# Kernel optimization log

Measured on AMD Instinct MI355X. Metric: run time of the kernel, lower is better.

## Reference

```python
import jax, jax.numpy as jnp
import numpy as np

N = 100000   # nodes
E = 1600000  # edges
IN = 512     # in_channels
H = 256      # hidden_channels
C = 40       # out_channels
BITS = 8     # INT8 fake quantization


def fake_quant(x, bits=BITS):
    """Symmetric per-tensor quantize-dequantize with straight-through estimator."""
    qmax = float(2 ** (bits - 1) - 1)
    scale = jnp.max(jnp.abs(x)) / qmax + 1e-12
    q = jnp.clip(jnp.round(x / scale), -qmax - 1.0, qmax) * scale
    # STE: forward = q, backward = identity
    return x + jax.lax.stop_gradient(q - x)


def quant_linear(x, w, b):
    # LinearQuantized: fake-quant inputs and weights, fp accumulate
    return fake_quant(x) @ fake_quant(w).T + b


def gcn_propagate(x, edge_index):
    """Symmetric-normalized sparse propagation: out = D^-1/2 A D^-1/2 x."""
    src, dst = edge_index[0], edge_index[1]
    deg = jax.ops.segment_sum(jnp.ones((E,), x.dtype), dst, num_segments=N)
    dinv = jnp.where(deg > 0, jax.lax.rsqrt(jnp.maximum(deg, 1.0)), 0.0)
    coef = dinv[src] * dinv[dst]                     # [E]
    msgs = x[src] * coef[:, None]                    # [E, C]
    return jax.ops.segment_sum(msgs, dst, num_segments=N)  # [N, C]


def setup_inputs() -> dict:
    key = jax.random.key(0)
    ks = jax.random.split(key, 6)
    x = jax.random.normal(ks[0], (N, IN), jnp.float32)
    edge_index = jax.random.randint(ks[1], (2, E), 0, N, dtype=jnp.int32)
    w1 = jax.random.normal(ks[2], (H, IN), jnp.float32) * (1.0 / np.sqrt(IN))
    b1 = jnp.zeros((H,), jnp.float32)
    w2 = jax.random.normal(ks[3], (C, H), jnp.float32) * (1.0 / np.sqrt(H))
    b2 = jnp.zeros((C,), jnp.float32)
    return {"x": x, "edge_index": edge_index, "w1": w1, "b1": b1, "w2": w2, "b2": b2}


def reference(x, edge_index, w1, b1, w2, b2):
    # dropout: identity in eval mode
    h = jax.nn.relu(quant_linear(x, w1, b1))         # [N, H]
    z = quant_linear(h, w2, b2)                      # [N, C]
    z = gcn_propagate(z, edge_index)                 # [N, C]
    return jax.nn.log_softmax(z, axis=1)
```

## Files before the change

### kernel.cpp

```cpp
#include <hip/hip_runtime.h>
#include <hip/hip_bf16.h>
#include <hip/hip_fp16.h>
#include <stdint.h>
#include <stddef.h>

#define NN   100000
#define NE   1600000
#define INC  512
#define HID  256
#define OC   40
#define OCP  48

#define LDS1 144
#define LDSB2 272

#define NBKT ((NN + 255) / 256)
#define NMT1 ((NN + 127) / 128)
#define GEMM1_BLKS (((NMT1 + 7) / 8) * 16)

#define ABS_X_BLKS  2048
#define ABS_W1_BLKS 128
#define ABS_W2_BLKS 16
#define ABS_TOT     (ABS_X_BLKS + ABS_W1_BLKS + ABS_W2_BLKS)
#define CHIST_BLKS  256
#define QW1_BLKS    128
#define QW2_BLKS    16
#define QW_TOT      (QW1_BLKS + QW2_BLKS)
#define BIN_BLOCKS  400
#define BIN_EPB     (NE / BIN_BLOCKS)

typedef float  f32x4  __attribute__((ext_vector_type(4)));
typedef int    i32x4  __attribute__((ext_vector_type(4)));
typedef _Float16 f16x8 __attribute__((ext_vector_type(8)));

__device__ unsigned g_amax_bits[4];
__device__ float    g_dinv[NN];
__device__ signed char g_qw1[HID * INC];
__device__ signed char g_qw2[OCP * HID];
__device__ _Float16 g_h[(size_t)NN * HID];
__device__ float    g_z[(size_t)NN * OC];
__device__ unsigned g_chist[NBKT];
__device__ unsigned g_cstart[NBKT + 1];
__device__ unsigned g_ccur[NBKT];
__device__ uint2    g_bin[NE];
__device__ unsigned g_rowstart[NN + 1];
__device__ int      g_csr_src[NE];

__device__ __forceinline__ float quantf(float v, float rs) {
    return fminf(fmaxf(rintf(v * rs), -128.0f), 127.0f);
}
__device__ __forceinline__ int pack4(float a, float b, float c, float d, float rs) {
    int q0 = (int)quantf(a, rs), q1 = (int)quantf(b, rs);
    int q2 = (int)quantf(c, rs), q3 = (int)quantf(d, rs);
    return (q0 & 255) | ((q1 & 255) << 8) | ((q2 & 255) << 16) | ((q3 & 255) << 24);
}
__device__ __forceinline__ i32x4 loadpack16(const float* p, float rs) {
    f32x4 v0 = *(const f32x4*)(p);
    f32x4 v1 = *(const f32x4*)(p + 4);
    f32x4 v2 = *(const f32x4*)(p + 8);
    f32x4 v3 = *(const f32x4*)(p + 12);
    i32x4 o;
    o[0] = pack4(v0.x, v0.y, v0.z, v0.w, rs);
    o[1] = pack4(v1.x, v1.y, v1.z, v1.w, rs);
    o[2] = pack4(v2.x, v2.y, v2.z, v2.w, rs);
    o[3] = pack4(v3.x, v3.y, v3.z, v3.w, rs);
    return o;
}

__global__ void init_kernel() {
    int idx = blockIdx.x * blockDim.x + threadIdx.x;
    int stride = gridDim.x * blockDim.x;
    for (int i = idx; i < NBKT; i += stride) g_chist[i] = 0u;
    for (int i = idx; i < (OCP * HID) / 4; i += stride) ((int*)g_qw2)[i] = 0;
    if (idx < 4) g_amax_bits[idx] = 0u;
}

__global__ void __launch_bounds__(256) absmax_chist_kernel(const float* __restrict__ x,
                                                           const float* __restrict__ w1,
                                                           const float* __restrict__ w2,
                                                           const int* __restrict__ ei) {
    __shared__ unsigned shist[NBKT];
    __shared__ float sm[4];
    int b = blockIdx.x;
    int t = threadIdx.x;
    if (b < ABS_TOT) {
        const float* src; int n4, slot, bbase, nb;
        if (b < ABS_X_BLKS) {
            src = x;  n4 = (NN * INC) / 4;  slot = 0; bbase = 0;                       nb = ABS_X_BLKS;
        } else if (b < ABS_X_BLKS + ABS_W1_BLKS) {
            src = w1; n4 = (HID * INC) / 4; slot = 1; bbase = ABS_X_BLKS;              nb = ABS_W1_BLKS;
        } else {
            src = w2; n4 = (OC * HID) / 4;  slot = 2; bbase = ABS_X_BLKS + ABS_W1_BLKS; nb = ABS_W2_BLKS;
        }
        int idx = (b - bbase) * 256 + t;
        int stride = nb * 256;
        const f32x4* s4 = (const f32x4*)src;
        float m = 0.0f;
        for (int i = idx; i < n4; i += stride) {
            f32x4 v = s4[i];
            m = fmaxf(m, fmaxf(fmaxf(fabsf(v.x), fabsf(v.y)),
                               fmaxf(fabsf(v.z), fabsf(v.w))));
        }
#pragma unroll
        for (int off = 32; off > 0; off >>= 1) m = fmaxf(m, __shfl_xor(m, off, 64));
        if ((t & 63) == 0) sm[t >> 6] = m;
        __syncthreads();
        if (t == 0) {
            float mm = fmaxf(fmaxf(sm[0], sm[1]), fmaxf(sm[2], sm[3]));
            atomicMax(&g_amax_bits[slot], __float_as_uint(mm));
        }
    } else {
        const int* dst = ei + NE;
        for (int i = t; i < NBKT; i += 256) shist[i] = 0u;
        __syncthreads();
        int idx = (b - ABS_TOT) * 256 + t;
        int stride = CHIST_BLKS * 256;
        for (int e = idx; e < NE; e += stride) atomicAdd(&shist[dst[e] >> 8], 1u);
        __syncthreads();
        for (int i = t; i < NBKT; i += 256) {
            unsigned c = shist[i];
            if (c) atomicAdd(&g_chist[i], c);
        }
    }
}

__global__ void cscan_kernel() {
    int t = threadIdx.x;
    unsigned v = (t < NBKT) ? g_chist[t] : 0u;
    int lane = t & 63, wv = t >> 6;
    unsigned sc = v;
#pragma unroll
    for (int off = 1; off < 64; off <<= 1) {
        unsigned n = __shfl_up(sc, off, 64);
        if (lane >= off) sc += n;
    }
    __shared__ unsigned ws[8];
    if (lane == 63) ws[wv] = sc;
    __syncthreads();
    unsigned woff = 0;
    for (int w = 0; w < 8; w++) if (w < wv) woff += ws[w];
    unsigned excl = woff + sc - v;
    if (t < NBKT) { g_cstart[t] = excl; g_ccur[t] = excl; }
    if (t == 0) g_cstart[NBKT] = NE;
}

__global__ void __launch_bounds__(256) quant_bin_kernel(const float* __restrict__ w1,
                                                        const float* __restrict__ w2,
                                                        const int* __restrict__ ei) {
    __shared__ unsigned hist[NBKT];
    __shared__ unsigned base[NBKT];
    int b = blockIdx.x;
    int t = threadIdx.x;
    if (b < QW_TOT) {
        const float* src; int* dst; int nint, slot, bbase, nb;
        if (b < QW1_BLKS) { src = w1; dst = (int*)g_qw1; nint = (HID * INC) / 4; slot = 1; bbase = 0;        nb = QW1_BLKS; }
        else              { src = w2; dst = (int*)g_qw2; nint = (OC * HID) / 4;  slot = 2; bbase = QW1_BLKS; nb = QW2_BLKS; }
        float rs = 1.0f / (__uint_as_float(g_amax_bits[slot]) / 127.0f + 1e-12f);
        int idx = (b - bbase) * 256 + t;
        int stride = nb * 256;
        for (int i = idx; i < nint; i += stride) {
            f32x4 v = *(const f32x4*)(src + (size_t)i * 4);
            dst[i] = pack4(v.x, v.y, v.z, v.w, rs);
        }
    } else {
        const int* srcp = ei;
        const int* dstp = ei + NE;
        int bb = b - QW_TOT;
        int e0 = bb * BIN_EPB, e1 = e0 + BIN_EPB;
        for (int i = t; i < NBKT; i += 256) hist[i] = 0u;
        __syncthreads();
        for (int e = e0 + t; e < e1; e += 256) atomicAdd(&hist[dstp[e] >> 8], 1u);
        __syncthreads();
        for (int i = t; i < NBKT; i += 256) {
            unsigned c = hist[i];
            base[i] = c ? atomicAdd(&g_ccur[i], c) : 0u;
            hist[i] = 0u;
        }
        __syncthreads();
        for (int e = e0 + t; e < e1; e += 256) {
            int d = dstp[e], s = srcp[e];
            int bk = d >> 8;
            unsigned r = atomicAdd(&hist[bk], 1u);
            g_bin[base[bk] + r] = make_uint2((unsigned)s, (unsigned)d);
        }
    }
}

__global__ void __launch_bounds__(256) gemm1_local_kernel(const float* __restrict__ x,
                                                          const float* __restrict__ b1) {
    __shared__ char lA[2][128 * LDS1];
    __shared__ char lB[2][128 * LDS1];
    int t = threadIdx.x;
    if (blockIdx.x >= GEMM1_BLKS) {
        int b = blockIdx.x - GEMM1_BLKS;
        unsigned* hist = (unsigned*)lA;
        unsigned* curs = hist + 256;
        unsigned* wsum = curs + 256;
        unsigned e0 = g_cstart[b], e1 = g_cstart[b + 1];
        hist[t] = 0u;
        __syncthreads();
        for (unsigned e = e0 + t; e < e1; e += 256) atomicAdd(&hist[g_bin[e].y & 255], 1u);
        __syncthreads();
        unsigned v = hist[t];
        int lane = t & 63, wv = t >> 6;
        unsigned sc = v;
#pragma unroll
        for (int off = 1; off < 64; off <<= 1) {
            unsigned n = __shfl_up(sc, off, 64);
            if (lane >= off) sc += n;
        }
        if (lane == 63) wsum[wv] = sc;
        __syncthreads();
        unsigned woff = 0;
        for (int w = 0; w < 4; w++) if (w < wv) woff += wsum[w];
        unsigned excl = woff + sc - v;
        int node = b * 256 + t;
        if (node < NN) {
            g_rowstart[node] = e0 + excl;
            g_dinv[node] = v ? rsqrtf((float)v) : 0.0f;
        }
        if (b == 0 && t == 0) g_rowstart[NN] = NE;
        curs[t] = excl;
        __syncthreads();
        for (unsigned e = e0 + t; e < e1; e += 256) {
            uint2 ed = g_bin[e];
            unsigned r = atomicAdd(&curs[ed.y & 255], 1u);
            g_csr_src[e0 + r] = (int)ed.x;
        }
        return;
    }
    int group = blockIdx.x >> 4;
    int ntile = (blockIdx.x >> 3) & 1;
    int mtile = group * 8 + (blockIdx.x & 7);
    if (mtile >= NMT1) return;
    int lane = t & 63, wv = t >> 6;
    int quad = lane >> 4, l16 = lane & 15;
    int mq = wv >> 1, nq = wv & 1;

    int srow = t >> 3;
    int sch  = t & 7;

    float rsx = 1.0f / (__uint_as_float(g_amax_bits[0]) / 127.0f + 1e-12f);

    const float* xb[4];
    const signed char* wb[4];
#pragma unroll
    for (int p = 0; p < 4; p++) {
        int gr = mtile * 128 + p * 32 + srow; if (gr >= NN) gr = NN - 1;
        xb[p] = x + (size_t)gr * INC + sch * 16;
        wb[p] = g_qw1 + (size_t)(ntile * 128 + p * 32 + srow) * INC + sch * 16;
    }

    i32x4 av[4], bv[4];
#pragma unroll
    for (int p = 0; p < 4; p++) {
        av[p] = loadpack16(xb[p], rsx);
        bv[p] = *(const i32x4*)(wb[p]);
    }

    i32x4 acc[4][4] = {};
#pragma unroll 1
    for (int kit = 0; kit < 4; kit++) {
        int bs = kit & 1;
#pragma unroll
        for (int p = 0; p < 4; p++) {
            int row = p * 32 + srow;
            *(i32x4*)(lA[bs] + row * LDS1 + sch * 16) = av[p];
            *(i32x4*)(lB[bs] + row * LDS1 + sch * 16) = bv[p];
        }
        if (kit + 1 < 4) {
#pragma unroll
            for (int p = 0; p < 4; p++) {
                av[p] = loadpack16(xb[p] + (kit + 1) * 128, rsx);
                bv[p] = *(const i32x4*)(wb[p] + (kit + 1) * 128);
            }
        }
        __syncthreads();
#pragma unroll
        for (int ks = 0; ks < 2; ks++) {
            int cs = ks * 64 + quad * 16;
            i32x4 a[4], b[4];
#pragma unroll
            for (int i = 0; i < 4; i++)
                a[i] = *(const i32x4*)(lA[bs] + (mq * 64 + i * 16 + l16) * LDS1 + cs);
#pragma unroll
            for (int j = 0; j < 4; j++)
                b[j] = *(const i32x4*)(lB[bs] + (nq * 64 + j * 16 + l16) * LDS1 + cs);
#pragma unroll
            for (int i = 0; i < 4; i++)
#pragma unroll
                for (int j = 0; j < 4; j++)
                    acc[i][j] = __builtin_amdgcn_mfma_i32_16x16x64_i8(a[i], b[j], acc[i][j], 0, 0, 0);
        }
    }
    float s = (__uint_as_float(g_amax_bits[0]) / 127.0f + 1e-12f)
            * (__uint_as_float(g_amax_bits[1]) / 127.0f + 1e-12f);
    float lmax = 0.0f;
#pragma unroll
    for (int j = 0; j < 4; j++) {
        int col = ntile * 128 + nq * 64 + j * 16 + l16;
        float bias = b1[col];
#pragma unroll
        for (int i = 0; i < 4; i++) {
#pragma unroll
            for (int r = 0; r < 4; r++) {
                int grow = mtile * 128 + mq * 64 + i * 16 + quad * 4 + r;
                float v = fmaxf(s * (float)acc[i][j][r] + bias, 0.0f);
                lmax = fmaxf(lmax, v);
                if (grow < NN) g_h[(size_t)grow * HID + col] = (_Float16)v;
            }
        }
    }
#pragma unroll
    for (int off = 32; off > 0; off >>= 1) lmax = fmaxf(lmax, __shfl_xor(lmax, off, 64));
    if (lane == 0) atomicMax(&g_amax_bits[3], __float_as_uint(lmax));
}

__launch_bounds__(256)
__global__ void gemm2_kernel(const float* __restrict__ b2) {
    __shared__ char lB2[OCP * LDSB2];
    __shared__ char lA2[128 * LDS1];
    int t = threadIdx.x;
    int mtile = blockIdx.x;
    int lane = t & 63, wv = t >> 6;
    int quad = lane >> 4, l16 = lane & 15;

#pragma unroll
    for (int p = 0; p < 3; p++) {
        int ci = p * 256 + t;
        int row = ci >> 4, ch = ci & 15;
        *(i32x4*)(lB2 + row * LDSB2 + ch * 16) =
            *(const i32x4*)(g_qw2 + row * 256 + ch * 16);
    }

    float scale_h = __uint_as_float(g_amax_bits[3]) / 127.0f + 1e-12f;
    float rs = 1.0f / scale_h;
    int srow = t >> 3, sch = t & 7;
    const _Float16* hbase[4];
#pragma unroll
    for (int p = 0; p < 4; p++) {
        int gr = mtile * 128 + p * 32 + srow; if (gr >= NN) gr = NN - 1;
        hbase[p] = g_h + (size_t)gr * HID + sch * 16;
    }

    i32x4 acc[2][3] = {};
#pragma unroll 1
    for (int kit = 0; kit < 2; kit++) {
        if (kit) __syncthreads();
#pragma unroll
        for (int p = 0; p < 4; p++) {
            int row = p * 32 + srow;
            const _Float16* hp = hbase[p] + kit * 128;
            f16x8 v0 = *(const f16x8*)(hp);
            f16x8 v1 = *(const f16x8*)(hp + 8);
            i32x4 o;
            o[0] = pack4((float)v0[0], (float)v0[1], (float)v0[2], (float)v0[3], rs);
            o[1] = pack4((float)v0[4], (float)v0[5], (float)v0[6], (float)v0[7], rs);
            o[2] = pack4((float)v1[0], (float)v1[1], (float)v1[2], (float)v1[3], rs);
            o[3] = pack4((float)v1[4], (float)v1[5], (float)v1[6], (float)v1[7], rs);
            *(i32x4*)(lA2 + row * LDS1 + sch * 16) = o;
        }
        __syncthreads();
#pragma unroll
        for (int ks = 0; ks < 2; ks++) {
            int cs = ks * 64 + quad * 16;
            i32x4 a[2], b[3];
#pragma unroll
            for (int i = 0; i < 2; i++)
                a[i] = *(const i32x4*)(lA2 + (wv * 32 + i * 16 + l16) * LDS1 + cs);
#pragma unroll
            for (int j = 0; j < 3; j++)
                b[j] = *(const i32x4*)(lB2 + (j * 16 + l16) * LDSB2 + kit * 128 + cs);
#pragma unroll
            for (int i = 0; i < 2; i++)
#pragma unroll
                for (int j = 0; j < 3; j++)
                    acc[i][j] = __builtin_amdgcn_mfma_i32_16x16x64_i8(a[i], b[j], acc[i][j], 0, 0, 0);
        }
    }
    float s = scale_h * (__uint_as_float(g_amax_bits[2]) / 127.0f + 1e-12f);
#pragma unroll
    for (int j = 0; j < 3; j++) {
        int col = j * 16 + l16;
        float bias = (col < OC) ? b2[col] : 0.0f;
#pragma unroll
        for (int i = 0; i < 2; i++) {
#pragma unroll
            for (int r = 0; r < 4; r++) {
                int grow = mtile * 128 + wv * 32 + i * 16 + quad * 4 + r;
                if (col < OC && grow < NN)
                    g_z[(size_t)grow * OC + col] = s * (float)acc[i][j][r] + bias;
            }
        }
    }
}

__launch_bounds__(256)
__global__ void gather_kernel(float* __restrict__ out) {
    int node = (blockIdx.x * 256 + threadIdx.x) >> 6;
    int lane = threadIdx.x & 63;
    if (node >= NN) return;
    unsigned e0 = g_rowstart[node], e1 = g_rowstart[node + 1];
    float dinvd = g_dinv[node];
    bool ch = (lane < OC);
    float acc0 = 0.0f, acc1 = 0.0f;
    unsigned e = e0;
    for (; e + 8 <= e1; e += 8) {
        int s0 = g_csr_src[e],     s1 = g_csr_src[e + 1];
        int s2 = g_csr_src[e + 2], s3 = g_csr_src[e + 3];
        int s4 = g_csr_src[e + 4], s5 = g_csr_src[e + 5];
        int s6 = g_csr_src[e + 6], s7 = g_csr_src[e + 7];
        float c0 = g_dinv[s0], c1 = g_dinv[s1], c2 = g_dinv[s2], c3 = g_dinv[s3];
        float c4 = g_dinv[s4], c5 = g_dinv[s5], c6 = g_dinv[s6], c7 = g_dinv[s7];
        float z0 = ch ? g_z[(size_t)s0 * OC + lane] : 0.0f;
        float z1 = ch ? g_z[(size_t)s1 * OC + lane] : 0.0f;
        float z2 = ch ? g_z[(size_t)s2 * OC + lane] : 0.0f;
        float z3 = ch ? g_z[(size_t)s3 * OC + lane] : 0.0f;
        float z4 = ch ? g_z[(size_t)s4 * OC + lane] : 0.0f;
        float z5 = ch ? g_z[(size_t)s5 * OC + lane] : 0.0f;
        float z6 = ch ? g_z[(size_t)s6 * OC + lane] : 0.0f;
        float z7 = ch ? g_z[(size_t)s7 * OC + lane] : 0.0f;
        acc0 += (z0 * c0 + z1 * c1) + (z2 * c2 + z3 * c3);
        acc1 += (z4 * c4 + z5 * c5) + (z6 * c6 + z7 * c7);
    }
    for (; e + 4 <= e1; e += 4) {
        int s0 = g_csr_src[e],     s1 = g_csr_src[e + 1];
        int s2 = g_csr_src[e + 2], s3 = g_csr_src[e + 3];
        float c0 = g_dinv[s0], c1 = g_dinv[s1], c2 = g_dinv[s2], c3 = g_dinv[s3];
        float z0 = ch ? g_z[(size_t)s0 * OC + lane] : 0.0f;
        float z1 = ch ? g_z[(size_t)s1 * OC + lane] : 0.0f;
        float z2 = ch ? g_z[(size_t)s2 * OC + lane] : 0.0f;
        float z3 = ch ? g_z[(size_t)s3 * OC + lane] : 0.0f;
        acc0 += (z0 * c0 + z1 * c1) + (z2 * c2 + z3 * c3);
    }
    for (; e < e1; e++) {
        int s0 = g_csr_src[e];
        float z0 = ch ? g_z[(size_t)s0 * OC + lane] : 0.0f;
        acc1 += z0 * g_dinv[s0];
    }
    float acc = (acc0 + acc1) * dinvd;
    float m = ch ? acc : -1e30f;
#pragma unroll
    for (int off = 32; off > 0; off >>= 1) m = fmaxf(m, __shfl_xor(m, off, 64));
    float ex = ch ? __expf(acc - m) : 0.0f;
    float ssum = ex;
#pragma unroll
    for (int off = 32; off > 0; off >>= 1) ssum += __shfl_xor(ssum, off, 64);
    float lg = __logf(ssum);
    if (ch) out[(size_t)node * OC + lane] = acc - m - lg;
}

extern "C" void kernel_launch(void* const* d_in, const int* in_sizes, int n_in,
                              void* d_out, int out_size, void* d_ws, size_t ws_size,
                              hipStream_t stream) {
    const float* x  = (const float*)d_in[0];
    const int*   ei = (const int*)d_in[1];
    const float* w1 = (const float*)d_in[2];
    const float* b1 = (const float*)d_in[3];
    const float* w2 = (const float*)d_in[4];
    const float* b2 = (const float*)d_in[5];
    float* out = (float*)d_out;
    (void)d_ws; (void)ws_size; (void)in_sizes; (void)n_in; (void)out_size;

    init_kernel<<<64, 256, 0, stream>>>();
    absmax_chist_kernel<<<ABS_TOT + CHIST_BLKS, 256, 0, stream>>>(x, w1, w2, ei);
    cscan_kernel<<<1, 512, 0, stream>>>();
    quant_bin_kernel<<<QW_TOT + BIN_BLOCKS, 256, 0, stream>>>(w1, w2, ei);
    gemm1_local_kernel<<<GEMM1_BLKS + NBKT, 256, 0, stream>>>(x, b1);
    gemm2_kernel<<<(NN + 127) / 128, 256, 0, stream>>>(b2);
    gather_kernel<<<(NN + 3) / 4, 256, 0, stream>>>(out);
}
```

Baseline: 546.3 us.

## Run gemm1 with 512 threads, single LDS buffer, and raw-float prefetch

The int8 GEMM1 kernel now launches 512 threads per block, with each wave computing a 32x64 output sub-tile instead of 64x64. Double-buffered LDS becomes a single buffer guarded by two barriers per k-step. Global loads now prefetch raw floats into registers and quantize them just before the LDS store, which lets loads overlap the MFMA work. The CSR-building blocks that share this kernel are adapted to 512 threads, with only the first 256 threads handling the histogram. This aims to raise occupancy and the number of outstanding memory requests, at the cost of extra barriers and more registers holding float prefetch data.

```diff
diff --git a/kernel.cpp b/kernel.cpp
--- a/kernel.cpp
+++ b/kernel.cpp
@@ -54,11 +54,7 @@
     int q2 = (int)quantf(c, rs), q3 = (int)quantf(d, rs);
     return (q0 & 255) | ((q1 & 255) << 8) | ((q2 & 255) << 16) | ((q3 & 255) << 24);
 }
-__device__ __forceinline__ i32x4 loadpack16(const float* p, float rs) {
-    f32x4 v0 = *(const f32x4*)(p);
-    f32x4 v1 = *(const f32x4*)(p + 4);
-    f32x4 v2 = *(const f32x4*)(p + 8);
-    f32x4 v3 = *(const f32x4*)(p + 12);
+__device__ __forceinline__ i32x4 pack16(f32x4 v0, f32x4 v1, f32x4 v2, f32x4 v3, float rs) {
     i32x4 o;
     o[0] = pack4(v0.x, v0.y, v0.z, v0.w, rs);
     o[1] = pack4(v1.x, v1.y, v1.z, v1.w, rs);
@@ -186,10 +182,10 @@
     }
 }
 
-__global__ void __launch_bounds__(256) gemm1_local_kernel(const float* __restrict__ x,
+__global__ void __launch_bounds__(512) gemm1_local_kernel(const float* __restrict__ x,
                                                           const float* __restrict__ b1) {
-    __shared__ char lA[2][128 * LDS1];
-    __shared__ char lB[2][128 * LDS1];
+    __shared__ char lA[128 * LDS1];
+    __shared__ char lB[128 * LDS1];
     int t = threadIdx.x;
     if (blockIdx.x >= GEMM1_BLKS) {
         int b = blockIdx.x - GEMM1_BLKS;
@@ -197,11 +193,11 @@
         unsigned* curs = hist + 256;
         unsigned* wsum = curs + 256;
         unsigned e0 = g_cstart[b], e1 = g_cstart[b + 1];
-        hist[t] = 0u;
-        __syncthreads();
-        for (unsigned e = e0 + t; e < e1; e += 256) atomicAdd(&hist[g_bin[e].y & 255], 1u);
-        __syncthreads();
-        unsigned v = hist[t];
+        if (t < 256) hist[t] = 0u;
+        __syncthreads();
+        for (unsigned e = e0 + t; e < e1; e += 512) atomicAdd(&hist[g_bin[e].y & 255], 1u);
+        __syncthreads();
+        unsigned v = (t < 256) ? hist[t] : 0u;
         int lane = t & 63, wv = t >> 6;
         unsigned sc = v;
 #pragma unroll
@@ -209,20 +205,20 @@
             unsigned n = __shfl_up(sc, off, 64);
             if (lane >= off) sc += n;
         }
-        if (lane == 63) wsum[wv] = sc;
+        if (lane == 63 && wv < 4) wsum[wv] = sc;
         __syncthreads();
         unsigned woff = 0;
         for (int w = 0; w < 4; w++) if (w < wv) woff += wsum[w];
         unsigned excl = woff + sc - v;
         int node = b * 256 + t;
-        if (node < NN) {
+        if (t < 256 && node < NN) {
             g_rowstart[node] = e0 + excl;
             g_dinv[node] = v ? rsqrtf((float)v) : 0.0f;
         }
         if (b == 0 && t == 0) g_rowstart[NN] = NE;
-        curs[t] = excl;
-        __syncthreads();
-        for (unsigned e = e0 + t; e < e1; e += 256) {
+        if (t < 256) curs[t] = excl;
+        __syncthreads();
+        for (unsigned e = e0 + t; e < e1; e += 512) {
             uint2 ed = g_bin[e];
             unsigned r = atomicAdd(&curs[ed.y & 255], 1u);
             g_csr_src[e0 + r] = (int)ed.x;
@@ -237,61 +233,55 @@
     int quad = lane >> 4, l16 = lane & 15;
     int mq = wv >> 1, nq = wv & 1;
 
-    int srow = t >> 3;
-    int sch  = t & 7;
+    int r = t >> 2, c = t & 3;
+    int gr = mtile * 128 + r; if (gr >= NN) gr = NN - 1;
+    const float* xp = x + (size_t)gr * INC + c * 32;
+    const signed char* wp = g_qw1 + (size_t)(ntile * 128 + r) * INC + c * 32;
+    char* lap = lA + r * LDS1 + c * 32;
+    char* lbp = lB + r * LDS1 + c * 32;
 
     float rsx = 1.0f / (__uint_as_float(g_amax_bits[0]) / 127.0f + 1e-12f);
 
-    const float* xb[4];
-    const signed char* wb[4];
-#pragma unroll
-    for (int p = 0; p < 4; p++) {
-        int gr = mtile * 128 + p * 32 + srow; if (gr >= NN) gr = NN - 1;
-        xb[p] = x + (size_t)gr * INC + sch * 16;
-        wb[p] = g_qw1 + (size_t)(ntile * 128 + p * 32 + srow) * INC + sch * 16;
-    }
-
-    i32x4 av[4], bv[4];
-#pragma unroll
-    for (int p = 0; p < 4; p++) {
-        av[p] = loadpack16(xb[p], rsx);
-        bv[p] = *(const i32x4*)(wb[p]);
-    }
-
-    i32x4 acc[4][4] = {};
+    f32x4 ra[8];
+    i32x4 rb[2];
+#pragma unroll
+    for (int k = 0; k < 8; k++) ra[k] = ((const f32x4*)xp)[k];
+#pragma unroll
+    for (int k = 0; k < 2; k++) rb[k] = ((const i32x4*)wp)[k];
+
+    i32x4 acc[2][4] = {};
 #pragma unroll 1
     for (int kit = 0; kit < 4; kit++) {
-        int bs = kit & 1;
-#pragma unroll
-        for (int p = 0; p < 4; p++) {
-            int row = p * 32 + srow;
-            *(i32x4*)(lA[bs] + row * LDS1 + sch * 16) = av[p];
-            *(i32x4*)(lB[bs] + row * LDS1 + sch * 16) = bv[p];
-        }
-        if (kit + 1 < 4) {
-#pragma unroll
-            for (int p = 0; p < 4; p++) {
-                av[p] = loadpack16(xb[p] + (kit + 1) * 128, rsx);
-                bv[p] = *(const i32x4*)(wb[p] + (kit + 1) * 128);
-            }
-        }
-        __syncthreads();
+        i32x4 oa0 = pack16(ra[0], ra[1], ra[2], ra[3], rsx);
+        i32x4 oa1 = pack16(ra[4], ra[5], ra[6], ra[7], rsx);
+        *(i32x4*)(lap)      = oa0;
+        *(i32x4*)(lap + 16) = oa1;
+        *(i32x4*)(lbp)      = rb[0];
+        *(i32x4*)(lbp + 16) = rb[1];
+        __syncthreads();
+        if (kit < 3) {
+#pragma unroll
+            for (int k = 0; k < 8; k++) ra[k] = ((const f32x4*)(xp + (kit + 1) * 128))[k];
+#pragma unroll
+            for (int k = 0; k < 2; k++) rb[k] = ((const i32x4*)(wp + (kit + 1) * 128))[k];
+        }
 #pragma unroll
         for (int ks = 0; ks < 2; ks++) {
             int cs = ks * 64 + quad * 16;
-            i32x4 a[4], b[4];
-#pragma unroll
-            for (int i = 0; i < 4; i++)
-                a[i] = *(const i32x4*)(lA[bs] + (mq * 64 + i * 16 + l16) * LDS1 + cs);
+            i32x4 a[2], b[4];
+#pragma unroll
+            for (int i = 0; i < 2; i++)
+                a[i] = *(const i32x4*)(lA + (mq * 32 + i * 16 + l16) * LDS1 + cs);
 #pragma unroll
             for (int j = 0; j < 4; j++)
-                b[j] = *(const i32x4*)(lB[bs] + (nq * 64 + j * 16 + l16) * LDS1 + cs);
-#pragma unroll
-            for (int i = 0; i < 4; i++)
+                b[j] = *(const i32x4*)(lB + (nq * 64 + j * 16 + l16) * LDS1 + cs);
+#pragma unroll
+            for (int i = 0; i < 2; i++)
 #pragma unroll
                 for (int j = 0; j < 4; j++)
                     acc[i][j] = __builtin_amdgcn_mfma_i32_16x16x64_i8(a[i], b[j], acc[i][j], 0, 0, 0);
         }
+        if (kit < 3) __syncthreads();
     }
     float s = (__uint_as_float(g_amax_bits[0]) / 127.0f + 1e-12f)
             * (__uint_as_float(g_amax_bits[1]) / 127.0f + 1e-12f);
@@ -301,11 +291,11 @@
         int col = ntile * 128 + nq * 64 + j * 16 + l16;
         float bias = b1[col];
 #pragma unroll
-        for (int i = 0; i < 4; i++) {
-#pragma unroll
-            for (int r = 0; r < 4; r++) {
-                int grow = mtile * 128 + mq * 64 + i * 16 + quad * 4 + r;
-                float v = fmaxf(s * (float)acc[i][j][r] + bias, 0.0f);
+        for (int i = 0; i < 2; i++) {
+#pragma unroll
+            for (int rr = 0; rr < 4; rr++) {
+                int grow = mtile * 128 + mq * 32 + i * 16 + quad * 4 + rr;
+                float v = fmaxf(s * (float)acc[i][j][rr] + bias, 0.0f);
                 lmax = fmaxf(lmax, v);
                 if (grow < NN) g_h[(size_t)grow * HID + col] = (_Float16)v;
             }
@@ -466,7 +456,7 @@
     absmax_chist_kernel<<<ABS_TOT + CHIST_BLKS, 256, 0, stream>>>(x, w1, w2, ei);
     cscan_kernel<<<1, 512, 0, stream>>>();
     quant_bin_kernel<<<QW_TOT + BIN_BLOCKS, 256, 0, stream>>>(w1, w2, ei);
-    gemm1_local_kernel<<<GEMM1_BLKS + NBKT, 256, 0, stream>>>(x, b1);
+    gemm1_local_kernel<<<GEMM1_BLKS + NBKT, 512, 0, stream>>>(x, b1);
     gemm2_kernel<<<(NN + 127) / 128, 256, 0, stream>>>(b2);
     gather_kernel<<<(NN + 3) / 4, 256, 0, stream>>>(out);
 }
```

Result: slower. 607.7 us (+11.2%).
